# Optimization experiments

Measured on AMD Instinct MI355X. Metric: run time of the kernel, lower is better.

Reference implementation:

```python
import jax, jax.numpy as jnp
import numpy as np

B, N, KNN_K = 4, 4096, 32
C1, C = 128, 256
K_SLOTS, RECON_M, N_RECON = 4, 96, 128
SLOT_ITERS = 3

def _ln(x, g, b):
    m = x.mean(-1, keepdims=True)
    v = jnp.var(x, axis=-1, keepdims=True)
    return (x - m) * jax.lax.rsqrt(v + 1e-5) * g + b

def _gather(f, idx):
    # f [B,P,C], idx [B,N,K] -> [B,N,K,C]
    return jax.vmap(lambda a, i: a[i])(f, idx)

def _knn(xyz, k):
    sq = jnp.sum(xyz * xyz, -1)
    d = sq[:, :, None] + sq[:, None, :] - 2.0 * jnp.einsum('bnc,bmc->bnm', xyz, xyz)
    return jax.lax.top_k(-d, k)[1]

def _conv_block(xyz, feats, W, b):
    # InterZPConv-style: KNN neighbor gather -> per-neighbor transform -> max aggregate
    idx = _knn(xyz, KNN_K)
    rel = _gather(xyz, idx) - xyz[:, :, None, :]
    h = jnp.concatenate([_gather(feats, idx), rel], axis=-1)
    h = jax.nn.relu(jnp.einsum('bnkc,cd->bnkd', h, W) + b)
    return h.max(axis=2)

def _bn(x, g, b):
    # BatchNorm2d (training mode) over (batch, slot) axes for 1x1-conv stacks
    m = x.mean(axis=(0, 1), keepdims=True)
    v = jnp.var(x, axis=(0, 1), keepdims=True)
    return (x - m) * jax.lax.rsqrt(v + 1e-5) * g + b

def _gru(upd, prev, W_ih, W_hh, b_ih, b_hh):
    gi = upd @ W_ih + b_ih
    gh = prev @ W_hh + b_hh
    r = jax.nn.sigmoid(gi[..., :C] + gh[..., :C])
    z = jax.nn.sigmoid(gi[..., C:2 * C] + gh[..., C:2 * C])
    n = jnp.tanh(gi[..., 2 * C:] + r * gh[..., 2 * C:])
    return (1.0 - z) * n + z * prev

def _chamfer(a, b):
    # a [B,M,3], b [B,P,3] -> (min over b per a-point, min over a per b-point), squared dists
    d = jnp.sum((a[..., :, None, :] - b[..., None, :, :]) ** 2, axis=-1)
    return d.min(axis=-1), d.min(axis=-2)

def _fps(pts):
    # farthest point sampling of N_RECON points from pts [P,3]
    P = pts.shape[0]
    d0 = jnp.full((P,), 1e10, pts.dtype)
    def step(carry, _):
        d, last = carry
        d = jnp.minimum(d, jnp.sum((pts - pts[last]) ** 2, axis=-1))
        nxt = jnp.argmax(d).astype(jnp.int32)
        return (d, nxt), nxt
    _, idxs = jax.lax.scan(step, (d0, jnp.array(0, jnp.int32)), None, length=N_RECON - 1)
    return jnp.concatenate([jnp.zeros((1,), jnp.int32), idxs])

def setup_inputs() -> dict:
    key = jax.random.key(0)
    ks = jax.random.split(key, 16)
    w = lambda k, s: jax.random.normal(k, s, jnp.float32) * 0.02
    z = lambda *s: jnp.zeros(s, jnp.float32)
    o = lambda *s: jnp.ones(s, jnp.float32)
    return {
        'x': jax.random.normal(ks[0], (B, 3, N), jnp.float32),
        'pose': jnp.zeros((B, N, 4, 4), jnp.float32),
        'W1': w(ks[1], (1 + 3, C1)), 'b1': z(C1),
        'W2': w(ks[2], (C1 + 3, C)), 'b2': z(C),
        'slots_mu': w(ks[3], (1, 1, C)), 'slots_sigma': jnp.abs(w(ks[4], (1, 1, C))) + 0.01,
        'ln_in_g': o(C), 'ln_in_b': z(C),
        'ln_slot_g': o(C), 'ln_slot_b': z(C),
        'ln_ff_g': o(C), 'ln_ff_b': z(C),
        'Wq': w(ks[5], (C, C)), 'Wk': w(ks[6], (C, C)), 'Wv': w(ks[7], (C, C)),
        'W_ih': w(ks[8], (C, 3 * C)), 'W_hh': w(ks[9], (C, 3 * C)),
        'b_ih': z(3 * C), 'b_hh': z(3 * C),
        'Wm1': w(ks[10], (C, C)), 'bm1': z(C),
        'Wm2': w(ks[11], (C, C)), 'bm2': z(C),
        'Wr1': w(ks[12], (C, C)), 'br1': z(C), 'g1': o(C), 'be1': z(C),
        'Wr2': w(ks[13], (C, C)), 'br2': z(C), 'g2': o(C), 'be2': z(C),
        'Wr3': w(ks[14], (C, RECON_M * 3)), 'br3': z(RECON_M * 3),
    }

def reference(x, pose, W1, b1, W2, b2, slots_mu, slots_sigma, ln_in_g, ln_in_b,
              ln_slot_g, ln_slot_b, ln_ff_g, ln_ff_b, Wq, Wk, Wv,
              W_ih, W_hh, b_ih, b_hh, Wm1, bm1, Wm2, bm2,
              Wr1, br1, g1, be1, Wr2, br2, g2, be2, Wr3, br3):
    xyz = jnp.transpose(x, (0, 2, 1))  # [B,N,3]
    feats = jnp.ones((B, N, 1), x.dtype)  # preprocess_input: unit features, na=1
    f = _conv_block(xyz, feats, W1, b1)   # [B,N,C1]
    f = _conv_block(xyz, f, W2, b2)       # [B,N,C]
    # Slot attention over per-point invariant features
    inp = _ln(f, ln_in_g, ln_in_b)
    kk = inp @ Wk
    vv = inp @ Wv
    slots = slots_mu + slots_sigma * jax.random.normal(jax.random.key(42), (B, K_SLOTS, C), x.dtype)
    scale = C ** -0.5
    attn = None
    for _ in range(SLOT_ITERS):
        prev = slots
        q = _ln(slots, ln_slot_g, ln_slot_b) @ Wq
        logits = scale * jnp.einsum('bkc,bnc->bkn', q, kk)
        attn = jax.nn.softmax(logits, axis=1)  # softmax over slots
        wgt = attn / (attn.sum(axis=-1, keepdims=True) + 1e-8)
        upd = jnp.einsum('bkn,bnc->bkc', wgt, vv)
        slots = _gru(upd, prev, W_ih, W_hh, b_ih, b_hh)
        h = _ln(slots, ln_ff_g, ln_ff_b)
        slots = slots + (jax.nn.relu(h @ Wm1 + bm1) @ Wm2 + bm2)
    attn_out = jnp.transpose(attn, (0, 2, 1))  # [B,N,K] (attn_ori.transpose(1,2))
    # Part reconstruction net (1x1 conv + BN + ReLU stack on slot features)
    h = jax.nn.relu(_bn(slots @ Wr1 + br1, g1, be1))
    h = jax.nn.relu(_bn(h @ Wr2 + br2, g2, be2))
    slot_points = (h @ Wr3 + br3).reshape(B, K_SLOTS, RECON_M, 3)
    all_pts = slot_points.reshape(B, K_SLOTS * RECON_M, 3)
    # FPS downsample + global chamfer against input points
    idx = jax.vmap(_fps)(all_pts)  # [B, N_RECON]
    ds = jnp.take_along_axis(all_pts, idx[..., None], axis=1)  # [B,N_RECON,3]
    d1, d2 = _chamfer(ds, xyz)
    loss = (d1.mean(-1) + d2.mean(-1)).mean()
    return loss, attn_out
```

## Files before the change

### kernel.cpp

```cpp
#include <hip/hip_runtime.h>

#define NBATCH 4
#define NPTS   4096
#define KNNK   32
#define C1D    128
#define CD     256
#define KPAD   160
#define ASTR   168
#define ASTR2  264

typedef _Float16 v8h __attribute__((ext_vector_type(8)));
typedef float    v4f __attribute__((ext_vector_type(4)));


__device__ __forceinline__ float block_sum256(float v, float* red) {
    #pragma unroll
    for (int o = 32; o; o >>= 1) v += __shfl_down(v, o);
    __syncthreads();
    if ((threadIdx.x & 63) == 0) red[threadIdx.x >> 6] = v;
    __syncthreads();
    return red[0] + red[1] + red[2] + red[3];
}

__device__ __forceinline__ unsigned rotl32(unsigned x, unsigned r) {
    return (x << r) | (x >> (32u - r));
}

__device__ float erfinv_f(float x) {
    float w = -log1pf(-x * x);
    float p;
    if (w < 5.0f) {
        w -= 2.5f;
        p = 2.81022636e-08f;
        p = fmaf(p, w, 3.43273939e-07f);
        p = fmaf(p, w, -3.5233877e-06f);
        p = fmaf(p, w, -4.39150654e-06f);
        p = fmaf(p, w, 0.00021858087f);
        p = fmaf(p, w, -0.00125372503f);
        p = fmaf(p, w, -0.00417768164f);
        p = fmaf(p, w, 0.246640727f);
        p = fmaf(p, w, 1.50140941f);
    } else {
        w = sqrtf(w) - 3.0f;
        p = -0.000200214257f;
        p = fmaf(p, w, 0.000100950558f);
        p = fmaf(p, w, 0.00134934322f);
        p = fmaf(p, w, -0.00367342844f);
        p = fmaf(p, w, 0.00573950773f);
        p = fmaf(p, w, -0.0076224613f);
        p = fmaf(p, w, 0.00943887047f);
        p = fmaf(p, w, 1.00167406f);
        p = fmaf(p, w, 2.83297682f);
    }
    return p * x;
}

__device__ __forceinline__ float bits_to_normal(unsigned bits) {
    unsigned fb = (bits >> 9) | 0x3f800000u;
    float f = __uint_as_float(fb) - 1.0f;
    const float lo = -0.99999994f;
    float u = fmaf(f, 2.0f, lo);
    u = fmaxf(u, lo);
    return 1.41421356237f * erfinv_f(u);
}

template <int CTRL, int RM>
__device__ __forceinline__ void dpp_lexmin(float& v, int& ix) {
    int tv = __builtin_amdgcn_update_dpp(__float_as_int(v), __float_as_int(v), CTRL, RM, 0xf, false);
    int ti = __builtin_amdgcn_update_dpp(ix, ix, CTRL, RM, 0xf, false);
    float fv = __int_as_float(tv);
    bool take = (fv < v) || (fv == v && ti < ix);
    v  = take ? fv : v;
    ix = take ? ti : ix;
}

template <int CTRL, int RM>
__device__ __forceinline__ void dpp_lexmax(float& v, int& ix) {
    int tv = __builtin_amdgcn_update_dpp(__float_as_int(v), __float_as_int(v), CTRL, RM, 0xf, false);
    int ti = __builtin_amdgcn_update_dpp(ix, ix, CTRL, RM, 0xf, false);
    float fv = __int_as_float(tv);
    bool take = (fv > v) || (fv == v && ti < ix);
    v  = take ? fv : v;
    ix = take ? ti : ix;
}


__global__ void prep_kernel(const float* __restrict__ x, float* __restrict__ xyz,
                            float4* __restrict__ xyzw) {
    int gid = blockIdx.x * 256 + threadIdx.x;
    if (gid >= NBATCH * NPTS) return;
    int b = gid >> 12, n = gid & (NPTS - 1);
    float a0 = x[(b * 3 + 0) * NPTS + n];
    float a1 = x[(b * 3 + 1) * NPTS + n];
    float a2 = x[(b * 3 + 2) * NPTS + n];
    xyz[gid * 3 + 0] = a0; xyz[gid * 3 + 1] = a1; xyz[gid * 3 + 2] = a2;
    float sq = a0 * a0 + a1 * a1 + a2 * a2;
    xyzw[gid] = make_float4(a0, a1, a2, sq);
}

__global__ void slots_init_kernel(const float* __restrict__ mu, const float* __restrict__ sg,
                                  float* __restrict__ slots) {
    int j = blockIdx.x * 256 + threadIdx.x;
    if (j >= 2048) return;
    unsigned ks0 = 0u, ks1 = 42u, ks2 = 0u ^ 42u ^ 0x1BD11BDAu;
    unsigned x0 = (unsigned)j + ks0;
    unsigned x1 = (unsigned)(j + 2048) + ks1;
    #define RND(r) { x0 += x1; x1 = rotl32(x1, r); x1 ^= x0; }
    RND(13u) RND(15u) RND(26u) RND(6u);  x0 += ks1; x1 += ks2 + 1u;
    RND(17u) RND(29u) RND(16u) RND(24u); x0 += ks2; x1 += ks0 + 2u;
    RND(13u) RND(15u) RND(26u) RND(6u);  x0 += ks0; x1 += ks1 + 3u;
    RND(17u) RND(29u) RND(16u) RND(24u); x0 += ks1; x1 += ks2 + 4u;
    RND(13u) RND(15u) RND(26u) RND(6u);  x0 += ks2; x1 += ks0 + 5u;
    #undef RND
    int c0 = j & 255, c1 = (j + 2048) & 255;
    slots[j]        = mu[c0] + sg[c0] * bits_to_normal(x0);
    slots[j + 2048] = mu[c1] + sg[c1] * bits_to_normal(x1);
}

__global__ __launch_bounds__(256) void knn_kernel(const float4* __restrict__ xyzw,
                                                  int* __restrict__ knn_idx) {
    int wid = threadIdx.x >> 6, lane = threadIdx.x & 63;
    int pid = blockIdx.x * 4 + wid;
    int b = pid >> 12, n = pid & (NPTS - 1);
    const float4* xb = xyzw + (size_t)b * NPTS;
    float4 p = xb[n];
    float d[64];
    #pragma unroll
    for (int i = 0; i < 64; ++i) {
        float4 c = xb[i * 64 + lane];
        float dot = p.x * c.x + p.y * c.y + p.z * c.z;
        d[i] = p.w + c.w - 2.0f * dot;
    }
    float gv[8]; int gi[8];
    #pragma unroll
    for (int g = 0; g < 8; ++g) {
        float mv = d[g * 8]; int mi = g * 8;
        #pragma unroll
        for (int j = 1; j < 8; ++j)
            if (d[g * 8 + j] < mv) { mv = d[g * 8 + j]; mi = g * 8 + j; }
        gv[g] = mv; gi[g] = mi * 64 + lane;
    }
    int* out = knn_idx + (size_t)pid * KNNK;
    #pragma unroll 1
    for (int s = 0; s < KNNK; ++s) {
        float bv = gv[0]; int bi = gi[0];
        #pragma unroll
        for (int g = 1; g < 8; ++g)
            if (gv[g] < bv) { bv = gv[g]; bi = gi[g]; }
        dpp_lexmin<0x111, 0xf>(bv, bi);
        dpp_lexmin<0x112, 0xf>(bv, bi);
        dpp_lexmin<0x114, 0xf>(bv, bi);
        dpp_lexmin<0x118, 0xf>(bv, bi);
        dpp_lexmin<0x142, 0xa>(bv, bi);
        dpp_lexmin<0x143, 0xc>(bv, bi);
        int fm = __builtin_amdgcn_readlane(bi, 63);
        if (lane == 0) out[s] = fm;
        int flane = fm & 63;
        int slot  = fm >> 6;
        if (lane == flane) {
            int g = slot >> 3;
            #pragma unroll
            for (int g2 = 0; g2 < 8; ++g2) {
                if (g2 == g) {
                    #pragma unroll
                    for (int j = 0; j < 8; ++j)
                        if (g2 * 8 + j == slot) d[g2 * 8 + j] = 1e30f;
                    float mv = d[g2 * 8]; int mi = g2 * 8;
                    #pragma unroll
                    for (int j = 1; j < 8; ++j)
                        if (d[g2 * 8 + j] < mv) { mv = d[g2 * 8 + j]; mi = g2 * 8 + j; }
                    gv[g2] = mv; gi[g2] = mi * 64 + lane;
                }
            }
        }
    }
}

__global__ __launch_bounds__(128) void conv1_kernel(const float* __restrict__ xyz,
                                                    const int* __restrict__ knn_idx,
                                                    const float* __restrict__ W1,
                                                    const float* __restrict__ b1,
                                                    _Float16* __restrict__ f1h) {
    int pid = blockIdx.x;
    int b = pid >> 12, n = pid & (NPTS - 1);
    int d = threadIdx.x;
    const float* xb = xyz + (size_t)b * NPTS * 3;
    float w0 = W1[d], wx = W1[C1D + d], wy = W1[2 * C1D + d], wz = W1[3 * C1D + d];
    float bb = b1[d];
    float px = xb[n * 3], py = xb[n * 3 + 1], pz = xb[n * 3 + 2];
    const int* idx = knn_idx + (size_t)pid * KNNK;
    float m = -1e30f;
    for (int k = 0; k < KNNK; ++k) {
        int j = idx[k];
        float rx = xb[j * 3] - px, ry = xb[j * 3 + 1] - py, rz = xb[j * 3 + 2] - pz;
        float v = w0 + bb + rx * wx + ry * wy + rz * wz;
        m = fmaxf(m, v);
    }
    f1h[(size_t)pid * C1D + d] = (_Float16)fmaxf(m, 0.0f);
}

__global__ void w2t_kernel(const float* __restrict__ W2, _Float16* __restrict__ W2t) {
    int n = blockIdx.x;
    int k = threadIdx.x;
    W2t[n * KPAD + k] = (k < 131) ? (_Float16)W2[k * CD + n] : (_Float16)0.0f;
}

__global__ void wkvt_kernel(const float* __restrict__ Wk, const float* __restrict__ Wv,
                            _Float16* __restrict__ WkvT) {
    int n = blockIdx.x;
    int c = threadIdx.x;
    float v = (n < 256) ? Wk[c * CD + n] : Wv[c * CD + (n - 256)];
    WkvT[n * CD + c] = (_Float16)v;
}

__global__ __launch_bounds__(256) void conv2_mfma_kernel(const float* __restrict__ xyz,
                                                         const _Float16* __restrict__ f1h,
                                                         const int* __restrict__ knn_idx,
                                                         const _Float16* __restrict__ W2t,
                                                         const float* __restrict__ b2,
                                                         const float* __restrict__ g_in,
                                                         const float* __restrict__ b_in,
                                                         _Float16* __restrict__ inph) {
    __shared__ _Float16 A[64 * ASTR];
    __shared__ float colmax[2 * CD];
    __shared__ float red[4];
    int pid2 = blockIdx.x;
    int gp0 = pid2 * 2;
    int b = gp0 >> 12, n0 = gp0 & (NPTS - 1);
    int tid = threadIdx.x;
    const int* idx = knn_idx + (size_t)pid2 * 64;
    const float* xb = xyz + (size_t)b * NPTS * 3;

    {
        int r = tid & 63, seg = tid >> 6;
        int j = idx[r];
        const uint4* s4 = (const uint4*)(f1h + ((size_t)b * NPTS + j) * C1D);
        uint4* d4 = (uint4*)&A[r * ASTR];
        #pragma unroll
        for (int i = 0; i < 4; ++i) d4[seg * 4 + i] = s4[seg * 4 + i];
        unsigned* z = (unsigned*)&A[r * ASTR + 128];
        for (int i = seg; i < 20; i += 4) z[i] = 0u;
        int np_ = (r < 32) ? n0 : (n0 + 1);
        if (seg == 0) {
            A[r * ASTR + 128] = (_Float16)(xb[j * 3 + 0] - xb[np_ * 3 + 0]);
            A[r * ASTR + 129] = (_Float16)(xb[j * 3 + 1] - xb[np_ * 3 + 1]);
        } else if (seg == 1) {
            A[r * ASTR + 130] = (_Float16)(xb[j * 3 + 2] - xb[np_ * 3 + 2]);
        }
    }
    __syncthreads();

    int w = tid >> 6, lane = tid & 63, quad = lane >> 4, lr = lane & 15;
    v4f acc[4][4];
    #pragma unroll
    for (int rt = 0; rt < 4; ++rt)
        #pragma unroll
        for (int ct = 0; ct < 4; ++ct)
            acc[rt][ct] = (v4f){0.0f, 0.0f, 0.0f, 0.0f};

    #pragma unroll
    for (int kk = 0; kk < KPAD; kk += 32) {
        v8h af[4], bf[4];
        #pragma unroll
        for (int rt = 0; rt < 4; ++rt)
            af[rt] = *(const v8h*)&A[(rt * 16 + lr) * ASTR + kk + quad * 8];
        #pragma unroll
        for (int ct = 0; ct < 4; ++ct) {
            int ncol = w * 64 + ct * 16 + lr;
            bf[ct] = *(const v8h*)(W2t + (size_t)ncol * KPAD + kk + quad * 8);
        }
        #pragma unroll
        for (int rt = 0; rt < 4; ++rt)
            #pragma unroll
            for (int ct = 0; ct < 4; ++ct)
                acc[rt][ct] = __builtin_amdgcn_mfma_f32_16x16x32_f16(af[rt], bf[ct], acc[rt][ct], 0, 0, 0);
    }

    #pragma unroll
    for (int ct = 0; ct < 4; ++ct) {
        float tm[4];
        #pragma unroll
        for (int rt = 0; rt < 4; ++rt) {
            v4f a = acc[rt][ct];
            float v = fmaxf(fmaxf(a[0], a[1]), fmaxf(a[2], a[3]));
            v = fmaxf(v, __shfl_xor(v, 16));
            v = fmaxf(v, __shfl_xor(v, 32));
            tm[rt] = v;
        }
        float p0 = fmaxf(tm[0], tm[1]);
        float p1 = fmaxf(tm[2], tm[3]);
        if (quad == 0) {
            colmax[0 * CD + w * 64 + ct * 16 + lr] = p0;
            colmax[1 * CD + w * 64 + ct * 16 + lr] = p1;
        }
    }
    __syncthreads();

    int d = tid;
    #pragma unroll
    for (int p = 0; p < 2; ++p) {
        float v = fmaxf(colmax[p * CD + d] + b2[d], 0.0f);
        float s = block_sum256(v, red);
        float mean = s * (1.0f / 256.0f);
        float s2 = block_sum256(v * v, red);
        float var = s2 * (1.0f / 256.0f) - mean * mean;
        float iv = (v - mean) * rsqrtf(var + 1e-5f) * g_in[d] + b_in[d];
        inph[(size_t)(gp0 + p) * CD + d] = (_Float16)iv;
    }
}

__global__ __launch_bounds__(256) void kv_mfma_kernel(const _Float16* __restrict__ inph,
                                                      const _Float16* __restrict__ WkvT,
                                                      float* __restrict__ kk,
                                                      float* __restrict__ vv) {
    __shared__ _Float16 A[64 * ASTR2];
    int rb = blockIdx.x >> 1, half = blockIdx.x & 1;
    int row0 = rb * 64;
    int tid = threadIdx.x;
    {
        const uint4* src4 = (const uint4*)(inph + (size_t)row0 * CD);
        #pragma unroll
        for (int i = 0; i < 8; ++i) {
            int idx = i * 256 + tid;
            int row = idx >> 5, c8 = idx & 31;
            *(uint4*)&A[row * ASTR2 + c8 * 8] = src4[idx];
        }
    }
    __syncthreads();
    int w = tid >> 6, lane = tid & 63, quad = lane >> 4, lr = lane & 15;
    v4f acc[4][4];
    #pragma unroll
    for (int rt = 0; rt < 4; ++rt)
        #pragma unroll
        for (int ct = 0; ct < 4; ++ct)
            acc[rt][ct] = (v4f){0.0f, 0.0f, 0.0f, 0.0f};
    #pragma unroll
    for (int ks = 0; ks < CD; ks += 32) {
        v8h af[4], bf[4];
        #pragma unroll
        for (int rt = 0; rt < 4; ++rt)
            af[rt] = *(const v8h*)&A[(rt * 16 + lr) * ASTR2 + ks + quad * 8];
        #pragma unroll
        for (int ct = 0; ct < 4; ++ct) {
            int ncol = half * 256 + w * 64 + ct * 16 + lr;
            bf[ct] = *(const v8h*)(WkvT + (size_t)ncol * CD + ks + quad * 8);
        }
        #pragma unroll
        for (int rt = 0; rt < 4; ++rt)
            #pragma unroll
            for (int ct = 0; ct < 4; ++ct)
                acc[rt][ct] = __builtin_amdgcn_mfma_f32_16x16x32_f16(af[rt], bf[ct], acc[rt][ct], 0, 0, 0);
    }
    float* dst = half ? vv : kk;
    #pragma unroll
    for (int rt = 0; rt < 4; ++rt)
        #pragma unroll
        for (int ct = 0; ct < 4; ++ct) {
            int col = w * 64 + ct * 16 + lr;
            #pragma unroll
            for (int r = 0; r < 4; ++r) {
                int row = rt * 16 + quad * 4 + r;
                dst[(size_t)(row0 + row) * CD + col] = acc[rt][ct][r];
            }
        }
}

__global__ __launch_bounds__(256) void slotq_kernel(const float* __restrict__ slots,
                                                    const float* __restrict__ g_sl,
                                                    const float* __restrict__ b_sl,
                                                    const float* __restrict__ Wq,
                                                    float* __restrict__ q,
                                                    float* __restrict__ asum) {
    int row = blockIdx.x;
    int d = threadIdx.x;
    __shared__ float sl[CD];
    __shared__ float red[4];
    float v = slots[row * CD + d];
    float s = block_sum256(v, red);
    float mean = s * (1.0f / 256.0f);
    float s2 = block_sum256(v * v, red);
    float var = s2 * (1.0f / 256.0f) - mean * mean;
    float ln = (v - mean) * rsqrtf(var + 1e-5f) * g_sl[d] + b_sl[d];
    sl[d] = ln;
    __syncthreads();
    float acc = 0.0f;
    const float4* sp = (const float4*)sl;
    for (int c4 = 0; c4 < 64; ++c4) {
        float4 x = sp[c4];
        int cb = c4 * 4;
        acc += x.x * Wq[cb * CD + d] + x.y * Wq[(cb + 1) * CD + d]
             + x.z * Wq[(cb + 2) * CD + d] + x.w * Wq[(cb + 3) * CD + d];
    }
    q[row * CD + d] = acc;
    if (row == 0 && d < 16) asum[d] = 0.0f;
}

__global__ __launch_bounds__(256) void attn_kernel(const float* __restrict__ q,
                                                   const float* __restrict__ kk,
                                                   float* __restrict__ attn,
                                                   float* __restrict__ asum,
                                                   float* __restrict__ out_attn) {
    int b = blockIdx.x >> 4;
    int nb = blockIdx.x & 15;
    int n = nb * 256 + threadIdx.x;
    __shared__ float qs[4 * CD];
    __shared__ float redk[16];
    for (int i = threadIdx.x; i < 4 * CD; i += 256) qs[i] = q[b * 4 * CD + i];
    __syncthreads();
    const float4* kp = (const float4*)(kk + ((size_t)b * NPTS + n) * CD);
    const float4* q0 = (const float4*)(qs);
    const float4* q1 = (const float4*)(qs + CD);
    const float4* q2 = (const float4*)(qs + 2 * CD);
    const float4* q3 = (const float4*)(qs + 3 * CD);
    float a0 = 0, a1 = 0, a2 = 0, a3 = 0;
    for (int c4 = 0; c4 < 64; ++c4) {
        float4 kv = kp[c4];
        float4 x;
        x = q0[c4]; a0 += kv.x * x.x + kv.y * x.y + kv.z * x.z + kv.w * x.w;
        x = q1[c4]; a1 += kv.x * x.x + kv.y * x.y + kv.z * x.z + kv.w * x.w;
        x = q2[c4]; a2 += kv.x * x.x + kv.y * x.y + kv.z * x.z + kv.w * x.w;
        x = q3[c4]; a3 += kv.x * x.x + kv.y * x.y + kv.z * x.z + kv.w * x.w;
    }
    const float scale = 0.0625f;
    float l0 = scale * a0, l1 = scale * a1, l2 = scale * a2, l3 = scale * a3;
    float mx = fmaxf(fmaxf(l0, l1), fmaxf(l2, l3));
    float e0 = expf(l0 - mx), e1 = expf(l1 - mx), e2 = expf(l2 - mx), e3 = expf(l3 - mx);
    float inv = 1.0f / (e0 + e1 + e2 + e3);
    e0 *= inv; e1 *= inv; e2 *= inv; e3 *= inv;
    attn[((size_t)b * 4 + 0) * NPTS + n] = e0;
    attn[((size_t)b * 4 + 1) * NPTS + n] = e1;
    attn[((size_t)b * 4 + 2) * NPTS + n] = e2;
    attn[((size_t)b * 4 + 3) * NPTS + n] = e3;
    if (out_attn) {
        float* o = out_attn + ((size_t)b * NPTS + n) * 4;
        o[0] = e0; o[1] = e1; o[2] = e2; o[3] = e3;
    }
    float as[4] = {e0, e1, e2, e3};
    #pragma unroll
    for (int k = 0; k < 4; ++k) {
        float v = as[k];
        #pragma unroll
        for (int o = 32; o; o >>= 1) v += __shfl_down(v, o);
        if ((threadIdx.x & 63) == 0) redk[(threadIdx.x >> 6) * 4 + k] = v;
    }
    __syncthreads();
    if (threadIdx.x < 4) {
        float s = redk[threadIdx.x] + redk[4 + threadIdx.x] + redk[8 + threadIdx.x] + redk[12 + threadIdx.x];
        atomicAdd(&asum[b * 4 + threadIdx.x], s);
    }
}

__global__ __launch_bounds__(256) void updp_kernel(const float* __restrict__ attn,
                                                   const float* __restrict__ vv,
                                                   float* __restrict__ updp) {
    int row = blockIdx.x >> 4, chunk = blockIdx.x & 15;
    int b = row >> 2;
    int d = threadIdx.x;
    const float* arow = attn + (size_t)row * NPTS + chunk * 256;
    const float* vb = vv + ((size_t)b * NPTS + chunk * 256) * CD;
    float acc = 0.0f;
    for (int n = 0; n < 256; ++n) acc += arow[n] * vb[(size_t)n * CD + d];
    updp[((size_t)row * 16 + chunk) * CD + d] = acc;
}

__global__ __launch_bounds__(256) void gru_gates_kernel(const float* __restrict__ updp,
                                                        const float* __restrict__ asum,
                                                        const float* __restrict__ slots,
                                                        const float* __restrict__ W_ih,
                                                        const float* __restrict__ W_hh,
                                                        const float* __restrict__ b_ih,
                                                        const float* __restrict__ b_hh,
                                                        float* __restrict__ gi,
                                                        float* __restrict__ gh) {
    int row = blockIdx.x / 3, gate = blockIdx.x % 3;
    int d = threadIdx.x;
    __shared__ float su[CD], sp[CD];
    float f = 1.0f / (asum[row] + 1e-8f);
    float u = 0.0f;
    for (int p = 0; p < 16; ++p) u += updp[((size_t)row * 16 + p) * CD + d];
    u *= f;
    su[d] = u; sp[d] = slots[row * CD + d];
    __syncthreads();
    float acc_i = b_ih[gate * CD + d];
    float acc_h = b_hh[gate * CD + d];
    const float* wi = W_ih + gate * CD + d;
    const float* wh = W_hh + gate * CD + d;
    for (int c = 0; c < CD; ++c) {
        acc_i += su[c] * wi[c * 3 * CD];
        acc_h += sp[c] * wh[c * 3 * CD];
    }
    gi[row * 3 * CD + gate * CD + d] = acc_i;
    gh[row * 3 * CD + gate * CD + d] = acc_h;
}

__global__ __launch_bounds__(256) void gru_mlp_kernel(const float* __restrict__ gi,
                                                      const float* __restrict__ gh,
                                                      float* __restrict__ slots,
                                                      const float* __restrict__ g_ff,
                                                      const float* __restrict__ b_ff,
                                                      const float* __restrict__ Wm1,
                                                      const float* __restrict__ bm1,
                                                      const float* __restrict__ Wm2,
                                                      const float* __restrict__ bm2) {
    int row = blockIdx.x;
    int d = threadIdx.x;
    __shared__ float sh[CD];
    __shared__ float red[4];
    float prev = slots[row * CD + d];
    float gir = gi[row * 3 * CD + d], giz = gi[row * 3 * CD + CD + d], gin = gi[row * 3 * CD + 2 * CD + d];
    float ghr = gh[row * 3 * CD + d], ghz = gh[row * 3 * CD + CD + d], ghn = gh[row * 3 * CD + 2 * CD + d];
    float r = 1.0f / (1.0f + expf(-(gir + ghr)));
    float z = 1.0f / (1.0f + expf(-(giz + ghz)));
    float nn = tanhf(gin + r * ghn);
    float sNew = (1.0f - z) * nn + z * prev;
    float s = block_sum256(sNew, red);
    float mean = s * (1.0f / 256.0f);
    float s2 = block_sum256(sNew * sNew, red);
    float var = s2 * (1.0f / 256.0f) - mean * mean;
    float h = (sNew - mean) * rsqrtf(var + 1e-5f) * g_ff[d] + b_ff[d];
    __syncthreads();
    sh[d] = h;
    __syncthreads();
    float y = bm1[d];
    {
        const float4* hp = (const float4*)sh;
        for (int c4 = 0; c4 < 64; ++c4) {
            float4 x = hp[c4];
            int cb = c4 * 4;
            y += x.x * Wm1[cb * CD + d] + x.y * Wm1[(cb + 1) * CD + d]
               + x.z * Wm1[(cb + 2) * CD + d] + x.w * Wm1[(cb + 3) * CD + d];
        }
    }
    y = fmaxf(y, 0.0f);
    __syncthreads();
    sh[d] = y;
    __syncthreads();
    float o = bm2[d];
    {
        const float4* hp = (const float4*)sh;
        for (int c4 = 0; c4 < 64; ++c4) {
            float4 x = hp[c4];
            int cb = c4 * 4;
            o += x.x * Wm2[cb * CD + d] + x.y * Wm2[(cb + 1) * CD + d]
               + x.z * Wm2[(cb + 2) * CD + d] + x.w * Wm2[(cb + 3) * CD + d];
        }
    }
    slots[row * CD + d] = sNew + o;
}

__global__ __launch_bounds__(320) void recon_kernel(const float* __restrict__ slots,
                                                    const float* __restrict__ Wr1, const float* __restrict__ br1,
                                                    const float* __restrict__ g1, const float* __restrict__ be1,
                                                    const float* __restrict__ Wr2, const float* __restrict__ br2,
                                                    const float* __restrict__ g2, const float* __restrict__ be2,
                                                    const float* __restrict__ Wr3, const float* __restrict__ br3,
                                                    float* __restrict__ spts) {
    __shared__ float sl[16 * CD];
    __shared__ float h1[16 * CD];
    __shared__ float h2[16 * CD];
    int d = threadIdx.x;
    if (d < CD) for (int r = 0; r < 16; ++r) sl[r * CD + d] = slots[r * CD + d];
    __syncthreads();
    if (d < CD) {
        float t[16];
        #pragma unroll
        for (int r = 0; r < 16; ++r) t[r] = br1[d];
        for (int c4 = 0; c4 < 64; ++c4) {
            int cb = c4 * 4;
            float w0 = Wr1[cb * CD + d], w1 = Wr1[(cb + 1) * CD + d];
            float w2 = Wr1[(cb + 2) * CD + d], w3 = Wr1[(cb + 3) * CD + d];
            #pragma unroll
            for (int r = 0; r < 16; ++r) {
                float4 x = *(const float4*)(sl + r * CD + cb);
                t[r] += x.x * w0 + x.y * w1 + x.z * w2 + x.w * w3;
            }
        }
        float mean = 0.0f;
        for (int r = 0; r < 16; ++r) mean += t[r];
        mean *= (1.0f / 16.0f);
        float var = 0.0f;
        for (int r = 0; r < 16; ++r) { float dd = t[r] - mean; var += dd * dd; }
        var *= (1.0f / 16.0f);
        float inv = rsqrtf(var + 1e-5f);
        for (int r = 0; r < 16; ++r)
            h1[r * CD + d] = fmaxf(0.0f, (t[r] - mean) * inv * g1[d] + be1[d]);
    }
    __syncthreads();
    if (d < CD) {
        float t[16];
        #pragma unroll
        for (int r = 0; r < 16; ++r) t[r] = br2[d];
        for (int c4 = 0; c4 < 64; ++c4) {
            int cb = c4 * 4;
            float w0 = Wr2[cb * CD + d], w1 = Wr2[(cb + 1) * CD + d];
            float w2 = Wr2[(cb + 2) * CD + d], w3 = Wr2[(cb + 3) * CD + d];
            #pragma unroll
            for (int r = 0; r < 16; ++r) {
                float4 x = *(const float4*)(h1 + r * CD + cb);
                t[r] += x.x * w0 + x.y * w1 + x.z * w2 + x.w * w3;
            }
        }
        float mean = 0.0f;
        for (int r = 0; r < 16; ++r) mean += t[r];
        mean *= (1.0f / 16.0f);
        float var = 0.0f;
        for (int r = 0; r < 16; ++r) { float dd = t[r] - mean; var += dd * dd; }
        var *= (1.0f / 16.0f);
        float inv = rsqrtf(var + 1e-5f);
        for (int r = 0; r < 16; ++r)
            h2[r * CD + d] = fmaxf(0.0f, (t[r] - mean) * inv * g2[d] + be2[d]);
    }
    __syncthreads();
    if (d < 288) {
        float t[16];
        #pragma unroll
        for (int r = 0; r < 16; ++r) t[r] = br3[d];
        for (int c4 = 0; c4 < 64; ++c4) {
            int cb = c4 * 4;
            float w0 = Wr3[cb * 288 + d], w1 = Wr3[(cb + 1) * 288 + d];
            float w2 = Wr3[(cb + 2) * 288 + d], w3 = Wr3[(cb + 3) * 288 + d];
            #pragma unroll
            for (int r = 0; r < 16; ++r) {
                float4 x = *(const float4*)(h2 + r * CD + cb);
                t[r] += x.x * w0 + x.y * w1 + x.z * w2 + x.w * w3;
            }
        }
        for (int r = 0; r < 16; ++r) spts[r * 288 + d] = t[r];
    }
}

__global__ __launch_bounds__(64) void fps_kernel(const float* __restrict__ spts,
                                                 int* __restrict__ fidx,
                                                 float* __restrict__ lacc,
                                                 unsigned* __restrict__ mnbuf) {
    int b = blockIdx.x;
    int lane = threadIdx.x;
    const float* pts = spts + (size_t)b * 384 * 3;
    int* out = fidx + b * 128;
    if (lane == 0) out[0] = 0;
    if (b == 0 && lane == 0) lacc[0] = 0.0f;
    mnbuf[b * 128 + lane] = 0x7F800000u;
    mnbuf[b * 128 + 64 + lane] = 0x7F800000u;
    float px[6], py[6], pz[6], dd[6];
    #pragma unroll
    for (int i = 0; i < 6; ++i) {
        int m = i * 64 + lane;
        px[i] = pts[m * 3]; py[i] = pts[m * 3 + 1]; pz[i] = pts[m * 3 + 2];
        dd[i] = 1e10f;
    }
    float lx = pts[0], ly = pts[1], lz = pts[2];
    #pragma unroll 1
    for (int s = 1; s < 128; ++s) {
        #pragma unroll
        for (int i = 0; i < 6; ++i) {
            float dx = px[i] - lx, dy = py[i] - ly, dz = pz[i] - lz;
            dd[i] = fminf(dd[i], dx * dx + dy * dy + dz * dz);
        }
        float bv = dd[0]; int bi = lane;
        #pragma unroll
        for (int i = 1; i < 6; ++i)
            if (dd[i] > bv) { bv = dd[i]; bi = i * 64 + lane; }
        dpp_lexmax<0x111, 0xf>(bv, bi);
        dpp_lexmax<0x112, 0xf>(bv, bi);
        dpp_lexmax<0x114, 0xf>(bv, bi);
        dpp_lexmax<0x118, 0xf>(bv, bi);
        dpp_lexmax<0x142, 0xa>(bv, bi);
        dpp_lexmax<0x143, 0xc>(bv, bi);
        int fm = __builtin_amdgcn_readlane(bi, 63);
        if (lane == 0) out[s] = fm;
        int slot = fm >> 6, sl_lane = fm & 63;
        float sx = px[0], sy = py[0], sz = pz[0];
        #pragma unroll
        for (int i = 1; i < 6; ++i)
            if (slot == i) { sx = px[i]; sy = py[i]; sz = pz[i]; }
        lx = __int_as_float(__builtin_amdgcn_readlane(__float_as_int(sx), sl_lane));
        ly = __int_as_float(__builtin_amdgcn_readlane(__float_as_int(sy), sl_lane));
        lz = __int_as_float(__builtin_amdgcn_readlane(__float_as_int(sz), sl_lane));
    }
}

__global__ __launch_bounds__(256) void chamfer_sum2_kernel(const float* __restrict__ spts,
                                                           const int* __restrict__ fidx,
                                                           const float* __restrict__ xyz,
                                                           float* __restrict__ lacc) {
    int b = blockIdx.x >> 4, chunk = blockIdx.x & 15;
    int t = threadIdx.x;
    __shared__ float ds[128 * 3];
    __shared__ float red[4];
    const float* pts = spts + (size_t)b * 384 * 3;
    if (t < 128) {
        int j = fidx[b * 128 + t];
        ds[t * 3] = pts[j * 3]; ds[t * 3 + 1] = pts[j * 3 + 1]; ds[t * 3 + 2] = pts[j * 3 + 2];
    }
    __syncthreads();
    int n = chunk * 256 + t;
    const float* xb = xyz + (size_t)b * NPTS * 3;
    float px = xb[n * 3], py = xb[n * 3 + 1], pz = xb[n * 3 + 2];
    float mn = 1e30f;
    #pragma unroll 4
    for (int jj = 0; jj < 128; ++jj) {
        float dx = ds[jj * 3] - px, dy = ds[jj * 3 + 1] - py, dz = ds[jj * 3 + 2] - pz;
        mn = fminf(mn, dx * dx + dy * dy + dz * dz);
    }
    float total = block_sum256(mn * (1.0f / 4096.0f), red);
    if (t == 0) atomicAdd(lacc, total);
}

__global__ __launch_bounds__(128) void chamfer_min1_kernel(const float* __restrict__ spts,
                                                           const int* __restrict__ fidx,
                                                           const float* __restrict__ xyz,
                                                           unsigned* __restrict__ mnbuf) {
    int b = blockIdx.x >> 4, chunk = blockIdx.x & 15;
    int t = threadIdx.x;
    __shared__ float tile[256 * 3];
    const float* xb = xyz + ((size_t)b * NPTS + chunk * 256) * 3;
    for (int i = t; i < 768; i += 128) tile[i] = xb[i];
    __syncthreads();
    int j = fidx[b * 128 + t];
    const float* pts = spts + (size_t)b * 384 * 3;
    float px = pts[j * 3], py = pts[j * 3 + 1], pz = pts[j * 3 + 2];
    float mn = 1e30f;
    #pragma unroll 4
    for (int i = 0; i < 256; ++i) {
        float dx = tile[i * 3] - px, dy = tile[i * 3 + 1] - py, dz = tile[i * 3 + 2] - pz;
        mn = fminf(mn, dx * dx + dy * dy + dz * dz);
    }
    atomicMin(&mnbuf[b * 128 + t], __float_as_uint(mn));
}

__global__ __launch_bounds__(512) void chamfer_final_kernel(const unsigned* __restrict__ mnbuf,
                                                            const float* __restrict__ lacc,
                                                            float* __restrict__ out) {
    int t = threadIdx.x;
    __shared__ float r[8];
    float v = __uint_as_float(mnbuf[t]) * (1.0f / 128.0f);
    #pragma unroll
    for (int o = 32; o; o >>= 1) v += __shfl_down(v, o);
    if ((t & 63) == 0) r[t >> 6] = v;
    __syncthreads();
    if (t == 0) {
        float tot = 0.0f;
        #pragma unroll
        for (int i = 0; i < 8; ++i) tot += r[i];
        out[0] = (lacc[0] + tot) * 0.25f;
    }
}


extern "C" void kernel_launch(void* const* d_in, const int* in_sizes, int n_in,
                              void* d_out, int out_size, void* d_ws, size_t ws_size,
                              hipStream_t stream) {
    (void)in_sizes; (void)n_in; (void)out_size; (void)ws_size;
    const float* x    = (const float*)d_in[0];
    const float* W1   = (const float*)d_in[2];
    const float* b1   = (const float*)d_in[3];
    const float* W2   = (const float*)d_in[4];
    const float* b2   = (const float*)d_in[5];
    const float* mu   = (const float*)d_in[6];
    const float* sg   = (const float*)d_in[7];
    const float* g_in = (const float*)d_in[8];
    const float* b_in = (const float*)d_in[9];
    const float* g_sl = (const float*)d_in[10];
    const float* b_sl = (const float*)d_in[11];
    const float* g_ff = (const float*)d_in[12];
    const float* b_ff = (const float*)d_in[13];
    const float* Wq   = (const float*)d_in[14];
    const float* Wk   = (const float*)d_in[15];
    const float* Wv   = (const float*)d_in[16];
    const float* W_ih = (const float*)d_in[17];
    const float* W_hh = (const float*)d_in[18];
    const float* b_ih = (const float*)d_in[19];
    const float* b_hh = (const float*)d_in[20];
    const float* Wm1  = (const float*)d_in[21];
    const float* bm1  = (const float*)d_in[22];
    const float* Wm2  = (const float*)d_in[23];
    const float* bm2  = (const float*)d_in[24];
    const float* Wr1  = (const float*)d_in[25];
    const float* br1  = (const float*)d_in[26];
    const float* g1   = (const float*)d_in[27];
    const float* be1  = (const float*)d_in[28];
    const float* Wr2  = (const float*)d_in[29];
    const float* br2  = (const float*)d_in[30];
    const float* g2   = (const float*)d_in[31];
    const float* be2  = (const float*)d_in[32];
    const float* Wr3  = (const float*)d_in[33];
    const float* br3  = (const float*)d_in[34];

    float* ws    = (float*)d_ws;
    float* xyz   = ws;
    float* xyzw  = xyz + 49152;
    int*   knn   = (int*)(xyzw + 65536);
    _Float16* f1h = (_Float16*)(knn + 524288);
    _Float16* W2t = (_Float16*)((float*)f1h + 1048576);
    _Float16* WkvT = (_Float16*)((float*)W2t + 20480);
    _Float16* inph = (_Float16*)((float*)WkvT + 65536);
    float* kkb   = (float*)inph + 2097152;
    float* vvb   = kkb + 4194304;
    float* slots = vvb + 4194304;
    float* qb    = slots + 4096;
    float* attn  = qb + 4096;
    float* asum  = attn + 65536;
    float* updp  = asum + 16;
    float* gi    = updp + 65536;
    float* gh    = gi + 12288;
    float* spts  = gh + 12288;
    int*   fidx  = (int*)(spts + 4608);
    float* lacc  = (float*)(fidx + 512);
    unsigned* mnbuf = (unsigned*)(lacc + 1);

    float* out = (float*)d_out;

    prep_kernel<<<64, 256, 0, stream>>>(x, xyz, (float4*)xyzw);
    slots_init_kernel<<<8, 256, 0, stream>>>(mu, sg, slots);
    knn_kernel<<<NBATCH * NPTS / 4, 256, 0, stream>>>((const float4*)xyzw, knn);
    conv1_kernel<<<NBATCH * NPTS, 128, 0, stream>>>(xyz, knn, W1, b1, f1h);
    w2t_kernel<<<256, 160, 0, stream>>>(W2, W2t);
    wkvt_kernel<<<512, 256, 0, stream>>>(Wk, Wv, WkvT);
    conv2_mfma_kernel<<<NBATCH * NPTS / 2, 256, 0, stream>>>(xyz, f1h, knn, W2t, b2, g_in, b_in, inph);
    kv_mfma_kernel<<<NBATCH * NPTS / 64 * 2, 256, 0, stream>>>(inph, WkvT, kkb, vvb);

    for (int it = 0; it < 3; ++it) {
        slotq_kernel<<<16, 256, 0, stream>>>(slots, g_sl, b_sl, Wq, qb, asum);
        attn_kernel<<<64, 256, 0, stream>>>(qb, kkb, attn, asum,
                                            (it == 2) ? (out + 1) : (float*)nullptr);
        updp_kernel<<<256, 256, 0, stream>>>(attn, vvb, updp);
        gru_gates_kernel<<<48, 256, 0, stream>>>(updp, asum, slots, W_ih, W_hh, b_ih, b_hh, gi, gh);
        gru_mlp_kernel<<<16, 256, 0, stream>>>(gi, gh, slots, g_ff, b_ff, Wm1, bm1, Wm2, bm2);
    }

    recon_kernel<<<1, 320, 0, stream>>>(slots, Wr1, br1, g1, be1, Wr2, br2, g2, be2, Wr3, br3, spts);
    fps_kernel<<<4, 64, 0, stream>>>(spts, fidx, lacc, mnbuf);
    chamfer_sum2_kernel<<<64, 256, 0, stream>>>(spts, fidx, xyz, lacc);
    chamfer_min1_kernel<<<64, 128, 0, stream>>>(spts, fidx, xyz, mnbuf);
    chamfer_final_kernel<<<1, 512, 0, stream>>>(mnbuf, lacc, out);
}
```

Baseline: 782.2 us.

## Fuse slot query, attention and weighted-value update into one kernel per iteration

Merges the slot LayerNorm+Wq projection, attention softmax, and attention-weighted value accumulation into a single kernel, keeping attention weights in shared memory instead of a global buffer. Each block redundantly recomputes q for its batch, and asum reset moves to init and the GRU MLP kernel. The KNN loop caches each lane's running minimum so it is only recomputed on the lane that lost its element, and conv1 loads neighbor coordinates once per lane and broadcasts them by shuffle. This removes launches and a global attn round-trip, but the fused update loop now runs 64 blocks over vv instead of 256, which lowers parallelism.

```diff
diff --git a/kernel.cpp b/kernel.cpp
--- a/kernel.cpp
+++ b/kernel.cpp
@@ -99,8 +99,9 @@
 }
 
 __global__ void slots_init_kernel(const float* __restrict__ mu, const float* __restrict__ sg,
-                                  float* __restrict__ slots) {
+                                  float* __restrict__ slots, float* __restrict__ asum) {
     int j = blockIdx.x * 256 + threadIdx.x;
+    if (j < 16) asum[j] = 0.0f;
     if (j >= 2048) return;
     unsigned ks0 = 0u, ks1 = 42u, ks2 = 0u ^ 42u ^ 0x1BD11BDAu;
     unsigned x0 = (unsigned)j + ks0;
@@ -140,13 +141,15 @@
             if (d[g * 8 + j] < mv) { mv = d[g * 8 + j]; mi = g * 8 + j; }
         gv[g] = mv; gi[g] = mi * 64 + lane;
     }
+    float lv = gv[0]; int li = gi[0];
+    #pragma unroll
+    for (int g = 1; g < 8; ++g)
+        if (gv[g] < lv) { lv = gv[g]; li = gi[g]; }
+
     int* out = knn_idx + (size_t)pid * KNNK;
     #pragma unroll 1
     for (int s = 0; s < KNNK; ++s) {
-        float bv = gv[0]; int bi = gi[0];
-        #pragma unroll
-        for (int g = 1; g < 8; ++g)
-            if (gv[g] < bv) { bv = gv[g]; bi = gi[g]; }
+        float bv = lv; int bi = li;
         dpp_lexmin<0x111, 0xf>(bv, bi);
         dpp_lexmin<0x112, 0xf>(bv, bi);
         dpp_lexmin<0x114, 0xf>(bv, bi);
@@ -172,6 +175,10 @@
                     gv[g2] = mv; gi[g2] = mi * 64 + lane;
                 }
             }
+            lv = gv[0]; li = gi[0];
+            #pragma unroll
+            for (int g2 = 1; g2 < 8; ++g2)
+                if (gv[g2] < lv) { lv = gv[g2]; li = gi[g2]; }
         }
     }
 }
@@ -183,17 +190,22 @@
                                                     _Float16* __restrict__ f1h) {
     int pid = blockIdx.x;
     int b = pid >> 12, n = pid & (NPTS - 1);
-    int d = threadIdx.x;
+    int d = threadIdx.x, lane = threadIdx.x & 63;
     const float* xb = xyz + (size_t)b * NPTS * 3;
     float w0 = W1[d], wx = W1[C1D + d], wy = W1[2 * C1D + d], wz = W1[3 * C1D + d];
     float bb = b1[d];
     float px = xb[n * 3], py = xb[n * 3 + 1], pz = xb[n * 3 + 2];
     const int* idx = knn_idx + (size_t)pid * KNNK;
+    float cx = 0.0f, cy = 0.0f, cz = 0.0f;
+    if (lane < 32) {
+        int j = idx[lane];
+        cx = xb[j * 3]; cy = xb[j * 3 + 1]; cz = xb[j * 3 + 2];
+    }
     float m = -1e30f;
+    #pragma unroll
     for (int k = 0; k < KNNK; ++k) {
-        int j = idx[k];
-        float rx = xb[j * 3] - px, ry = xb[j * 3 + 1] - py, rz = xb[j * 3 + 2] - pz;
-        float v = w0 + bb + rx * wx + ry * wy + rz * wz;
+        float jx = __shfl(cx, k), jy = __shfl(cy, k), jz = __shfl(cz, k);
+        float v = w0 + bb + (jx - px) * wx + (jy - py) * wy + (jz - pz) * wz;
         m = fmaxf(m, v);
     }
     f1h[(size_t)pid * C1D + d] = (_Float16)fmaxf(m, 0.0f);
@@ -365,48 +377,56 @@
         }
 }
 
-__global__ __launch_bounds__(256) void slotq_kernel(const float* __restrict__ slots,
-                                                    const float* __restrict__ g_sl,
-                                                    const float* __restrict__ b_sl,
-                                                    const float* __restrict__ Wq,
-                                                    float* __restrict__ q,
-                                                    float* __restrict__ asum) {
-    int row = blockIdx.x;
-    int d = threadIdx.x;
-    __shared__ float sl[CD];
+__global__ __launch_bounds__(256) void slot_attn_kernel(const float* __restrict__ slots,
+                                                        const float* __restrict__ g_sl,
+                                                        const float* __restrict__ b_sl,
+                                                        const float* __restrict__ Wq,
+                                                        const float* __restrict__ kk,
+                                                        const float* __restrict__ vv,
+                                                        float* __restrict__ asum,
+                                                        float* __restrict__ updp,
+                                                        float* __restrict__ out_attn) {
+    int b = blockIdx.x >> 4;
+    int chunk = blockIdx.x & 15;
+    int t = threadIdx.x;
+    __shared__ float sl[4 * CD];
+    __shared__ float qs[4 * CD];
+    __shared__ float aw[256 * 4];
     __shared__ float red[4];
-    float v = slots[row * CD + d];
-    float s = block_sum256(v, red);
-    float mean = s * (1.0f / 256.0f);
-    float s2 = block_sum256(v * v, red);
-    float var = s2 * (1.0f / 256.0f) - mean * mean;
-    float ln = (v - mean) * rsqrtf(var + 1e-5f) * g_sl[d] + b_sl[d];
-    sl[d] = ln;
-    __syncthreads();
-    float acc = 0.0f;
-    const float4* sp = (const float4*)sl;
-    for (int c4 = 0; c4 < 64; ++c4) {
-        float4 x = sp[c4];
-        int cb = c4 * 4;
-        acc += x.x * Wq[cb * CD + d] + x.y * Wq[(cb + 1) * CD + d]
-             + x.z * Wq[(cb + 2) * CD + d] + x.w * Wq[(cb + 3) * CD + d];
-    }
-    q[row * CD + d] = acc;
-    if (row == 0 && d < 16) asum[d] = 0.0f;
-}
-
-__global__ __launch_bounds__(256) void attn_kernel(const float* __restrict__ q,
-                                                   const float* __restrict__ kk,
-                                                   float* __restrict__ attn,
-                                                   float* __restrict__ asum,
-                                                   float* __restrict__ out_attn) {
-    int b = blockIdx.x >> 4;
-    int nb = blockIdx.x & 15;
-    int n = nb * 256 + threadIdx.x;
-    __shared__ float qs[4 * CD];
     __shared__ float redk[16];
-    for (int i = threadIdx.x; i < 4 * CD; i += 256) qs[i] = q[b * 4 * CD + i];
-    __syncthreads();
+
+    #pragma unroll 1
+    for (int r = 0; r < 4; ++r) {
+        float v = slots[(b * 4 + r) * CD + t];
+        float s = block_sum256(v, red);
+        float mean = s * (1.0f / 256.0f);
+        float s2 = block_sum256(v * v, red);
+        float var = s2 * (1.0f / 256.0f) - mean * mean;
+        sl[r * CD + t] = (v - mean) * rsqrtf(var + 1e-5f) * g_sl[t] + b_sl[t];
+    }
+    __syncthreads();
+    {
+        float a0 = 0.0f, a1 = 0.0f, a2 = 0.0f, a3 = 0.0f;
+        const float4* s0 = (const float4*)(sl);
+        const float4* s1 = (const float4*)(sl + CD);
+        const float4* s2p = (const float4*)(sl + 2 * CD);
+        const float4* s3 = (const float4*)(sl + 3 * CD);
+        for (int c4 = 0; c4 < 64; ++c4) {
+            int cb = c4 * 4;
+            float w0 = Wq[cb * CD + t], w1 = Wq[(cb + 1) * CD + t];
+            float w2 = Wq[(cb + 2) * CD + t], w3 = Wq[(cb + 3) * CD + t];
+            float4 x0 = s0[c4], x1 = s1[c4], x2 = s2p[c4], x3 = s3[c4];
+            a0 += x0.x * w0 + x0.y * w1 + x0.z * w2 + x0.w * w3;
+            a1 += x1.x * w0 + x1.y * w1 + x1.z * w2 + x1.w * w3;
+            a2 += x2.x * w0 + x2.y * w1 + x2.z * w2 + x2.w * w3;
+            a3 += x3.x * w0 + x3.y * w1 + x3.z * w2 + x3.w * w3;
+        }
+        qs[0 * CD + t] = a0; qs[1 * CD + t] = a1;
+        qs[2 * CD + t] = a2; qs[3 * CD + t] = a3;
+    }
+    __syncthreads();
+
+    int n = chunk * 256 + t;
     const float4* kp = (const float4*)(kk + ((size_t)b * NPTS + n) * CD);
     const float4* q0 = (const float4*)(qs);
     const float4* q1 = (const float4*)(qs + CD);
@@ -427,10 +447,7 @@
     float e0 = expf(l0 - mx), e1 = expf(l1 - mx), e2 = expf(l2 - mx), e3 = expf(l3 - mx);
     float inv = 1.0f / (e0 + e1 + e2 + e3);
     e0 *= inv; e1 *= inv; e2 *= inv; e3 *= inv;
-    attn[((size_t)b * 4 + 0) * NPTS + n] = e0;
-    attn[((size_t)b * 4 + 1) * NPTS + n] = e1;
-    attn[((size_t)b * 4 + 2) * NPTS + n] = e2;
-    attn[((size_t)b * 4 + 3) * NPTS + n] = e3;
+    aw[t * 4 + 0] = e0; aw[t * 4 + 1] = e1; aw[t * 4 + 2] = e2; aw[t * 4 + 3] = e3;
     if (out_attn) {
         float* o = out_attn + ((size_t)b * NPTS + n) * 4;
         o[0] = e0; o[1] = e1; o[2] = e2; o[3] = e3;
@@ -441,26 +458,25 @@
         float v = as[k];
         #pragma unroll
         for (int o = 32; o; o >>= 1) v += __shfl_down(v, o);
-        if ((threadIdx.x & 63) == 0) redk[(threadIdx.x >> 6) * 4 + k] = v;
-    }
-    __syncthreads();
-    if (threadIdx.x < 4) {
-        float s = redk[threadIdx.x] + redk[4 + threadIdx.x] + redk[8 + threadIdx.x] + redk[12 + threadIdx.x];
-        atomicAdd(&asum[b * 4 + threadIdx.x], s);
-    }
-}
-
-__global__ __launch_bounds__(256) void updp_kernel(const float* __restrict__ attn,
-                                                   const float* __restrict__ vv,
-                                                   float* __restrict__ updp) {
-    int row = blockIdx.x >> 4, chunk = blockIdx.x & 15;
-    int b = row >> 2;
-    int d = threadIdx.x;
-    const float* arow = attn + (size_t)row * NPTS + chunk * 256;
+        if ((t & 63) == 0) redk[(t >> 6) * 4 + k] = v;
+    }
+    __syncthreads();
+    if (t < 4) {
+        float s = redk[t] + redk[4 + t] + redk[8 + t] + redk[12 + t];
+        atomicAdd(&asum[b * 4 + t], s);
+    }
+
+    float ac0 = 0.0f, ac1 = 0.0f, ac2 = 0.0f, ac3 = 0.0f;
     const float* vb = vv + ((size_t)b * NPTS + chunk * 256) * CD;
-    float acc = 0.0f;
-    for (int n = 0; n < 256; ++n) acc += arow[n] * vb[(size_t)n * CD + d];
-    updp[((size_t)row * 16 + chunk) * CD + d] = acc;
+    for (int nn2 = 0; nn2 < 256; ++nn2) {
+        float v = vb[(size_t)nn2 * CD + t];
+        float4 w4 = *(const float4*)&aw[nn2 * 4];
+        ac0 += w4.x * v; ac1 += w4.y * v; ac2 += w4.z * v; ac3 += w4.w * v;
+    }
+    updp[((size_t)(b * 4 + 0) * 16 + chunk) * CD + t] = ac0;
+    updp[((size_t)(b * 4 + 1) * 16 + chunk) * CD + t] = ac1;
+    updp[((size_t)(b * 4 + 2) * 16 + chunk) * CD + t] = ac2;
+    updp[((size_t)(b * 4 + 3) * 16 + chunk) * CD + t] = ac3;
 }
 
 __global__ __launch_bounds__(256) void gru_gates_kernel(const float* __restrict__ updp,
@@ -501,7 +517,8 @@
                                                       const float* __restrict__ Wm1,
                                                       const float* __restrict__ bm1,
                                                       const float* __restrict__ Wm2,
-                                                      const float* __restrict__ bm2) {
+                                                      const float* __restrict__ bm2,
+                                                      float* __restrict__ asum) {
     int row = blockIdx.x;
     int d = threadIdx.x;
     __shared__ float sh[CD];
@@ -509,6 +526,7 @@
     float prev = slots[row * CD + d];
     float gir = gi[row * 3 * CD + d], giz = gi[row * 3 * CD + CD + d], gin = gi[row * 3 * CD + 2 * CD + d];
     float ghr = gh[row * 3 * CD + d], ghz = gh[row * 3 * CD + CD + d], ghn = gh[row * 3 * CD + 2 * CD + d];
+    if (d == 0) asum[row] = 0.0f;
     float r = 1.0f / (1.0f + expf(-(gir + ghr)));
     float z = 1.0f / (1.0f + expf(-(giz + ghz)));
     float nn = tanhf(gin + r * ghn);
@@ -797,9 +815,7 @@
     float* kkb   = (float*)inph + 2097152;
     float* vvb   = kkb + 4194304;
     float* slots = vvb + 4194304;
-    float* qb    = slots + 4096;
-    float* attn  = qb + 4096;
-    float* asum  = attn + 65536;
+    float* asum  = slots + 4096;
     float* updp  = asum + 16;
     float* gi    = updp + 65536;
     float* gh    = gi + 12288;
@@ -811,7 +827,7 @@
     float* out = (float*)d_out;
 
     prep_kernel<<<64, 256, 0, stream>>>(x, xyz, (float4*)xyzw);
-    slots_init_kernel<<<8, 256, 0, stream>>>(mu, sg, slots);
+    slots_init_kernel<<<8, 256, 0, stream>>>(mu, sg, slots, asum);
     knn_kernel<<<NBATCH * NPTS / 4, 256, 0, stream>>>((const float4*)xyzw, knn);
     conv1_kernel<<<NBATCH * NPTS, 128, 0, stream>>>(xyz, knn, W1, b1, f1h);
     w2t_kernel<<<256, 160, 0, stream>>>(W2, W2t);
@@ -820,12 +836,10 @@
     kv_mfma_kernel<<<NBATCH * NPTS / 64 * 2, 256, 0, stream>>>(inph, WkvT, kkb, vvb);
 
     for (int it = 0; it < 3; ++it) {
-        slotq_kernel<<<16, 256, 0, stream>>>(slots, g_sl, b_sl, Wq, qb, asum);
-        attn_kernel<<<64, 256, 0, stream>>>(qb, kkb, attn, asum,
-                                            (it == 2) ? (out + 1) : (float*)nullptr);
-        updp_kernel<<<256, 256, 0, stream>>>(attn, vvb, updp);
+        slot_attn_kernel<<<64, 256, 0, stream>>>(slots, g_sl, b_sl, Wq, kkb, vvb, asum, updp,
+                                                 (it == 2) ? (out + 1) : (float*)nullptr);
         gru_gates_kernel<<<48, 256, 0, stream>>>(updp, asum, slots, W_ih, W_hh, b_ih, b_hh, gi, gh);
-        gru_mlp_kernel<<<16, 256, 0, stream>>>(gi, gh, slots, g_ff, b_ff, Wm1, bm1, Wm2, bm2);
+        gru_mlp_kernel<<<16, 256, 0, stream>>>(gi, gh, slots, g_ff, b_ff, Wm1, bm1, Wm2, bm2, asum);
     }
 
     recon_kernel<<<1, 320, 0, stream>>>(slots, Wr1, br1, g1, be1, Wr2, br2, g2, be2, Wr3, br3, spts);
```

Measured after the change: 786.2 us. Within noise of the previous version (+0.5%).
